# Optimization experiments

Hardware: AMD Instinct MI355X
Metric: run time of the kernel (lower is better)

Reference implementation:

```python
import jax, jax.numpy as jnp
import numpy as np
from itertools import product

_EPS = 1e-5
N_VOX = 120000
C = 64
B, D, H, Wd = 2, 400, 400, 40  # batch and spatial voxel grid


def _build_rulebook(seed=0):
    """Random unique active voxels + [N,27] submanifold neighbor index table (-1 = inactive)."""
    rng = np.random.default_rng(seed)
    size = B * D * H * Wd
    flat = rng.choice(size, size=N_VOX, replace=False)
    b = flat // (D * H * Wd)
    rem = flat % (D * H * Wd)
    z = rem // (H * Wd)
    rem2 = rem % (H * Wd)
    y = rem2 // Wd
    x = rem2 % Wd
    lut = np.full(size, -1, np.int32)
    lut[flat] = np.arange(N_VOX, dtype=np.int32)
    offs = np.array(list(product([-1, 0, 1], repeat=3)), dtype=np.int64)  # [27,3]
    zz = z[:, None] + offs[None, :, 0]
    yy = y[:, None] + offs[None, :, 1]
    xx = x[:, None] + offs[None, :, 2]
    valid = (zz >= 0) & (zz < D) & (yy >= 0) & (yy < H) & (xx >= 0) & (xx < Wd)
    nf = ((b[:, None] * D + zz) * H + yy) * Wd + xx
    nbr = np.where(valid, lut[np.clip(nf, 0, size - 1)], -1).astype(np.int32)
    return nbr


def setup_inputs() -> dict:
    key = jax.random.key(0)
    ks = jax.random.split(key, 12)
    nbr = jnp.asarray(_build_rulebook())
    return {
        "features": jax.random.normal(ks[0], (N_VOX, C), jnp.float32),
        "W1": jax.random.normal(ks[1], (27, C, C), jnp.float32) * 0.05,
        "g1": jax.random.uniform(ks[2], (C,), jnp.float32, 0.5, 1.5),
        "b1": jax.random.normal(ks[3], (C,), jnp.float32) * 0.1,
        "m1": jax.random.normal(ks[4], (C,), jnp.float32) * 0.1,
        "v1": jax.random.uniform(ks[5], (C,), jnp.float32, 0.5, 1.5),
        "W2": jax.random.normal(ks[6], (27, C, C), jnp.float32) * 0.05,
        "g2": jax.random.uniform(ks[7], (C,), jnp.float32, 0.5, 1.5),
        "b2": jax.random.normal(ks[8], (C,), jnp.float32) * 0.1,
        "m2": jax.random.normal(ks[9], (C,), jnp.float32) * 0.1,
        "v2": jax.random.uniform(ks[10], (C,), jnp.float32, 0.5, 1.5),
        "nbr_idx": nbr,
    }


def _subm_conv(f, nbr, W):
    # gather-GEMM: f [N,Cin], nbr [N,27], W [27,Cin,Cout] -> [N,Cout]
    mask = (nbr >= 0)[:, :, None]
    g = jnp.where(mask, f[jnp.clip(nbr, 0)], jnp.zeros((), f.dtype))  # [N,27,Cin]
    return jnp.einsum('nkc,kcd->nd', g, W)


def _bn(x, g, b, m, v):
    return (x - m) * (g * jax.lax.rsqrt(v + _EPS)) + b


def reference(features, W1, g1, b1, m1, v1, W2, g2, b2, m2, v2, nbr_idx):
    out = _bn(_subm_conv(features, nbr_idx, W1), g1, b1, m1, v1)
    out = jax.nn.relu(out)
    out = _bn(_subm_conv(out, nbr_idx, W2), g2, b2, m2, v2)
    return jax.nn.relu(out + features)
```

## Files before the change

kernel.cpp:

```cpp
#include <hip/hip_runtime.h>

typedef short short8 __attribute__((ext_vector_type(8)));
typedef float f32x4 __attribute__((ext_vector_type(4)));

#define N_VOX 120000
#define C64 64
#define K27 27
#define KC 13
#define TILES 3750
#define CAPT 64
#define LAYER_W 110592

#define WS_TCNT 0
#define WS_BNP  16384
#define WS_PWC  20480
#define WS_PWV  40960
#define WS_ENTS 524288
#define WS_MIDB (4u << 20)

__device__ __forceinline__ ushort f2bf(float x) {
    uint u = __float_as_uint(x);
    u = (u + 0x7FFFu + ((u >> 16) & 1u)) >> 16;
    return (ushort)u;
}
__device__ __forceinline__ float bf2f(ushort u) {
    return __uint_as_float((uint)u << 16);
}

__global__ __launch_bounds__(256) void prep_kernel(const float* __restrict__ W1,
                                                   const float* __restrict__ W2,
                                                   const float* g1, const float* b1,
                                                   const float* m1, const float* v1,
                                                   const float* g2, const float* b2,
                                                   const float* m2, const float* v2,
                                                   ushort* __restrict__ pwv,
                                                   ushort* __restrict__ pwc,
                                                   int* __restrict__ tcnt,
                                                   float* __restrict__ bnp) {
    int tid = blockIdx.x * 256 + threadIdx.x;
    if (tid < 221184) {
        int L = tid / LAYER_W, r = tid % LAYER_W;
        const float* W = L ? W2 : W1;
        pwv[tid] = f2bf(W[r]);
    } else if (tid < 229376) {
        int j2 = tid - 221184;
        int L = j2 >> 12, q = j2 & 4095;
        int ks = q >> 11, tq = (q >> 9) & 3, ln = (q >> 3) & 63, jj = q & 7;
        int c = ks * 32 + (ln >> 4) * 8 + jj;
        int d = tq * 16 + (ln & 15);
        const float* W = L ? W2 : W1;
        pwc[L * 4096 + q] = f2bf(W[(size_t)KC * 4096 + c * 64 + d]);
    } else if (tid < 233126) {
        tcnt[tid - 229376] = 0;
    } else if (tid < 233190) {
        int i = tid - 233126;
        float s1 = g1[i] * rsqrtf(v1[i] + 1e-5f);
        bnp[i] = s1; bnp[64 + i] = b1[i] - m1[i] * s1;
        float s2 = g2[i] * rsqrtf(v2[i] + 1e-5f);
        bnp[128 + i] = s2; bnp[192 + i] = b2[i] - m2[i] * s2;
    }
}

__global__ __launch_bounds__(256) void build_csr_kernel(const int* __restrict__ nbr,
                                                        int* __restrict__ tcnt,
                                                        int2* __restrict__ ents) {
    int n = blockIdx.x * 256 + threadIdx.x;
    if (n >= N_VOX) return;
    const int* row = nbr + (size_t)n * K27;
    const int tile = n >> 5, nl = n & 31;
#pragma unroll
    for (int k = 0; k < K27; ++k) {
        if (k == KC) continue;
        int m = row[k];
        if (m >= 0) {
            int slot = atomicAdd(&tcnt[tile], 1);
            if (slot < CAPT) ents[tile * CAPT + slot] = make_int2(nl | (k << 8), m);
        }
    }
}

template <bool LAYER2>
__global__ __launch_bounds__(64) void fused_layer_kernel(const float* __restrict__ f,
                                                         const ushort* __restrict__ midb_in,
                                                         const ushort* __restrict__ pwc,
                                                         const ushort* __restrict__ pwv,
                                                         const int* __restrict__ tcnt,
                                                         const int2* __restrict__ ents,
                                                         const float* __restrict__ bnp,
                                                         ushort* __restrict__ midb_out,
                                                         float* __restrict__ fout) {
    __shared__ float ext[32 * C64];
    const int lane = threadIdx.x;
    const int tile = blockIdx.x;
    const int n0 = tile * 32;
    const int r16 = lane & 15, kg = lane >> 4;

#pragma unroll
    for (int i = 0; i < 8; ++i) ((f32x4*)ext)[i * 64 + lane] = (f32x4)0.f;

    const short8* B = (const short8*)pwc;
    short8 Bf[2][4];
#pragma unroll
    for (int s = 0; s < 2; ++s)
#pragma unroll
        for (int t = 0; t < 4; ++t) Bf[s][t] = B[(s * 4 + t) * 64 + lane];

    f32x4 acc[2][4];
#pragma unroll
    for (int v = 0; v < 2; ++v)
#pragma unroll
        for (int t = 0; t < 4; ++t) acc[v][t] = (f32x4)0.f;

#pragma unroll
    for (int v = 0; v < 2; ++v) {
        short8 a0, a1;
        if (LAYER2) {
            const short8* ar = (const short8*)(midb_in + (size_t)(n0 + v * 16 + r16) * C64);
            a0 = ar[kg];
            a1 = ar[4 + kg];
        } else {
            const float4* ar = (const float4*)(f + (size_t)(n0 + v * 16 + r16) * C64);
            float4 fa = ar[kg * 2], fb = ar[kg * 2 + 1];
            float4 fc = ar[8 + kg * 2], fd = ar[9 + kg * 2];
            a0[0] = f2bf(fa.x); a0[1] = f2bf(fa.y); a0[2] = f2bf(fa.z); a0[3] = f2bf(fa.w);
            a0[4] = f2bf(fb.x); a0[5] = f2bf(fb.y); a0[6] = f2bf(fb.z); a0[7] = f2bf(fb.w);
            a1[0] = f2bf(fc.x); a1[1] = f2bf(fc.y); a1[2] = f2bf(fc.z); a1[3] = f2bf(fc.w);
            a1[4] = f2bf(fd.x); a1[5] = f2bf(fd.y); a1[6] = f2bf(fd.z); a1[7] = f2bf(fd.w);
        }
#pragma unroll
        for (int t = 0; t < 4; ++t) {
            acc[v][t] = __builtin_amdgcn_mfma_f32_16x16x32_bf16(a0, Bf[0][t], acc[v][t], 0, 0, 0);
            acc[v][t] = __builtin_amdgcn_mfma_f32_16x16x32_bf16(a1, Bf[1][t], acc[v][t], 0, 0, 0);
        }
    }

    int cnt = tcnt[tile];
    cnt = cnt > CAPT ? CAPT : cnt;
    for (int p = 0; p < cnt; ++p) {
        int2 e = ents[tile * CAPT + p];
        int nl = __builtin_amdgcn_readfirstlane(e.x & 255);
        int k  = __builtin_amdgcn_readfirstlane(e.x >> 8);
        int m  = __builtin_amdgcn_readfirstlane(e.y);
        const ushort* wk = pwv + (size_t)k * 4096 + lane;
        float ee = 0.f;
        if (LAYER2) {
            const ushort* am = midb_in + (size_t)m * C64;
#pragma unroll
            for (int c = 0; c < C64; ++c)
                ee = fmaf(bf2f(am[c]), bf2f(wk[c * 64]), ee);
        } else {
            const float* am = f + (size_t)m * C64;
#pragma unroll
            for (int c = 0; c < C64; ++c)
                ee = fmaf(am[c], bf2f(wk[c * 64]), ee);
        }
        ext[nl * C64 + lane] += ee;
    }

    float s[4], h[4];
#pragma unroll
    for (int t = 0; t < 4; ++t) {
        s[t] = bnp[t * 16 + r16];
        h[t] = bnp[64 + t * 16 + r16];
    }
#pragma unroll
    for (int v = 0; v < 2; ++v)
#pragma unroll
        for (int t = 0; t < 4; ++t)
#pragma unroll
            for (int r = 0; r < 4; ++r) {
                const int row = v * 16 + kg * 4 + r;
                const int ch = t * 16 + r16;
                float val = acc[v][t][r] + ext[row * C64 + ch];
                val = fmaf(val, s[t], h[t]);
                if (LAYER2) {
                    val += f[(size_t)(n0 + row) * C64 + ch];
                    fout[(size_t)(n0 + row) * C64 + ch] = fmaxf(val, 0.f);
                } else {
                    midb_out[(size_t)(n0 + row) * C64 + ch] = f2bf(fmaxf(val, 0.f));
                }
            }
}

extern "C" void kernel_launch(void* const* d_in, const int* in_sizes, int n_in,
                              void* d_out, int out_size, void* d_ws, size_t ws_size,
                              hipStream_t stream) {
    const float* f   = (const float*)d_in[0];
    const float* W1  = (const float*)d_in[1];
    const float* g1  = (const float*)d_in[2];
    const float* b1  = (const float*)d_in[3];
    const float* m1  = (const float*)d_in[4];
    const float* v1  = (const float*)d_in[5];
    const float* W2  = (const float*)d_in[6];
    const float* g2  = (const float*)d_in[7];
    const float* b2  = (const float*)d_in[8];
    const float* m2  = (const float*)d_in[9];
    const float* v2  = (const float*)d_in[10];
    const int*   nbr = (const int*)d_in[11];
    float* out = (float*)d_out;

    char* ws = (char*)d_ws;
    int*    tcnt = (int*)(ws + WS_TCNT);
    float*  bnp  = (float*)(ws + WS_BNP);
    ushort* pwc  = (ushort*)(ws + WS_PWC);
    ushort* pwv  = (ushort*)(ws + WS_PWV);
    int2*   ents = (int2*)(ws + WS_ENTS);
    ushort* midb = (ushort*)(ws + WS_MIDB);

    prep_kernel<<<911, 256, 0, stream>>>(W1, W2, g1, b1, m1, v1, g2, b2, m2, v2,
                                         pwv, pwc, tcnt, bnp);
    build_csr_kernel<<<(N_VOX + 255) / 256, 256, 0, stream>>>(nbr, tcnt, ents);

    fused_layer_kernel<false><<<TILES, 64, 0, stream>>>(
        f, nullptr, pwc, pwv, tcnt, ents, bnp, midb, nullptr);
    fused_layer_kernel<true><<<TILES, 64, 0, stream>>>(
        f, midb, pwc + 4096, pwv + LAYER_W, tcnt, ents, bnp + 128, nullptr, out);
}
```

Baseline: 183.5 us.

## Merge prep and CSR build, use LDS atomics, vectorize gathers and epilogue

Prep and CSR build now run in one launch. Each wave builds its tile's entry list with shared-memory atomics in place of global atomics, so the counter array no longer needs zeroing. The off-center weights are stored transposed, so each lane reads contiguous short8 rows, and the scalar dot product is split across four accumulators. The fused layer kernels pack four tiles per 256-thread block, and the epilogue goes through LDS so stores are coalesced float4/short8 writes. The risks are higher LDS use per block (32 KB), which limits occupancy, and more register pressure.

New measurement: 205.4 us. 1.12x slower.

```diff
diff --git a/kernel.cpp b/kernel.cpp
--- a/kernel.cpp
+++ b/kernel.cpp
@@ -10,11 +10,14 @@
 #define TILES 3750
 #define CAPT 64
 #define LAYER_W 110592
+#define CSRB 938
+#define PACKB 65
+#define FUSEB 938
 
 #define WS_TCNT 0
 #define WS_BNP  16384
 #define WS_PWC  20480
-#define WS_PWV  40960
+#define WS_PWT  40960
 #define WS_ENTS 524288
 #define WS_MIDB (4u << 20)
 
@@ -27,76 +30,84 @@
     return __uint_as_float((uint)u << 16);
 }
 
-__global__ __launch_bounds__(256) void prep_kernel(const float* __restrict__ W1,
-                                                   const float* __restrict__ W2,
-                                                   const float* g1, const float* b1,
-                                                   const float* m1, const float* v1,
-                                                   const float* g2, const float* b2,
-                                                   const float* m2, const float* v2,
-                                                   ushort* __restrict__ pwv,
-                                                   ushort* __restrict__ pwc,
-                                                   int* __restrict__ tcnt,
-                                                   float* __restrict__ bnp) {
-    int tid = blockIdx.x * 256 + threadIdx.x;
-    if (tid < 221184) {
-        int L = tid / LAYER_W, r = tid % LAYER_W;
-        const float* W = L ? W2 : W1;
-        pwv[tid] = f2bf(W[r]);
-    } else if (tid < 229376) {
-        int j2 = tid - 221184;
-        int L = j2 >> 12, q = j2 & 4095;
-        int ks = q >> 11, tq = (q >> 9) & 3, ln = (q >> 3) & 63, jj = q & 7;
-        int c = ks * 32 + (ln >> 4) * 8 + jj;
-        int d = tq * 16 + (ln & 15);
-        const float* W = L ? W2 : W1;
-        pwc[L * 4096 + q] = f2bf(W[(size_t)KC * 4096 + c * 64 + d]);
-    } else if (tid < 233126) {
-        tcnt[tid - 229376] = 0;
-    } else if (tid < 233190) {
-        int i = tid - 233126;
-        float s1 = g1[i] * rsqrtf(v1[i] + 1e-5f);
-        bnp[i] = s1; bnp[64 + i] = b1[i] - m1[i] * s1;
-        float s2 = g2[i] * rsqrtf(v2[i] + 1e-5f);
-        bnp[128 + i] = s2; bnp[192 + i] = b2[i] - m2[i] * s2;
-    }
-}
-
-__global__ __launch_bounds__(256) void build_csr_kernel(const int* __restrict__ nbr,
-                                                        int* __restrict__ tcnt,
-                                                        int2* __restrict__ ents) {
-    int n = blockIdx.x * 256 + threadIdx.x;
-    if (n >= N_VOX) return;
-    const int* row = nbr + (size_t)n * K27;
-    const int tile = n >> 5, nl = n & 31;
-#pragma unroll
-    for (int k = 0; k < K27; ++k) {
-        if (k == KC) continue;
-        int m = row[k];
-        if (m >= 0) {
-            int slot = atomicAdd(&tcnt[tile], 1);
-            if (slot < CAPT) ents[tile * CAPT + slot] = make_int2(nl | (k << 8), m);
-        }
-    }
-}
-
-template <bool LAYER2>
-__global__ __launch_bounds__(64) void fused_layer_kernel(const float* __restrict__ f,
-                                                         const ushort* __restrict__ midb_in,
-                                                         const ushort* __restrict__ pwc,
-                                                         const ushort* __restrict__ pwv,
-                                                         const int* __restrict__ tcnt,
-                                                         const int2* __restrict__ ents,
-                                                         const float* __restrict__ bnp,
-                                                         ushort* __restrict__ midb_out,
-                                                         float* __restrict__ fout) {
-    __shared__ float ext[32 * C64];
-    const int lane = threadIdx.x;
-    const int tile = blockIdx.x;
+__global__ __launch_bounds__(256) void prep_csr_kernel(
+    const int* __restrict__ nbr,
+    const float* __restrict__ W1, const float* __restrict__ W2,
+    const float* g1, const float* b1, const float* m1, const float* v1,
+    const float* g2, const float* b2, const float* m2, const float* v2,
+    int* __restrict__ tcnt, int2* __restrict__ ents,
+    ushort* __restrict__ pwt, ushort* __restrict__ pwc,
+    float* __restrict__ bnp) {
+    if (blockIdx.x < CSRB) {
+        __shared__ int cnt_[4];
+        const int wv = threadIdx.x >> 6, lane = threadIdx.x & 63;
+        const int tile = blockIdx.x * 4 + wv;
+        const bool act = tile < TILES;
+        if (lane == 0) cnt_[wv] = 0;
+        __syncthreads();
+        if (act) {
+            const int base = tile * (32 * K27);
+            for (int e = lane; e < 32 * K27; e += 64) {
+                const int k = e % K27;
+                if (k == KC) continue;
+                const int m = nbr[base + e];
+                if (m >= 0) {
+                    const int nl = e / K27;
+                    int slot = atomicAdd(&cnt_[wv], 1);
+                    if (slot < CAPT) ents[tile * CAPT + slot] = make_int2(nl | (k << 8), m);
+                }
+            }
+        }
+        __syncthreads();
+        if (act && lane == 0) {
+            int c = cnt_[wv];
+            tcnt[tile] = c > CAPT ? CAPT : c;
+        }
+    } else {
+        int idx = (blockIdx.x - CSRB) * 256 + threadIdx.x;
+        const int stride = PACKB * 256;
+        for (; idx < 229440; idx += stride) {
+            if (idx < 221184) {
+                int L = idx / LAYER_W, r = idx % LAYER_W;
+                int k = r >> 12, dc = r & 4095, d = dc >> 6, c = dc & 63;
+                const float* W = L ? W2 : W1;
+                pwt[idx] = f2bf(W[(size_t)k * 4096 + c * 64 + d]);
+            } else if (idx < 229376) {
+                int j2 = idx - 221184;
+                int L = j2 >> 12, q = j2 & 4095;
+                int ks = q >> 11, tq = (q >> 9) & 3, ln = (q >> 3) & 63, jj = q & 7;
+                int c = ks * 32 + (ln >> 4) * 8 + jj;
+                int d = tq * 16 + (ln & 15);
+                const float* W = L ? W2 : W1;
+                pwc[L * 4096 + q] = f2bf(W[(size_t)KC * 4096 + c * 64 + d]);
+            } else {
+                int i = idx - 229376;
+                float s1 = g1[i] * rsqrtf(v1[i] + 1e-5f);
+                bnp[i] = s1; bnp[64 + i] = b1[i] - m1[i] * s1;
+                float s2 = g2[i] * rsqrtf(v2[i] + 1e-5f);
+                bnp[128 + i] = s2; bnp[192 + i] = b2[i] - m2[i] * s2;
+            }
+        }
+    }
+}
+
+template <bool L2P>
+__device__ __forceinline__ void fused_core(const float* __restrict__ f,
+                                           const ushort* __restrict__ midin,
+                                           const ushort* __restrict__ pwc,
+                                           const ushort* __restrict__ pwt,
+                                           const int* __restrict__ tcnt,
+                                           const int2* __restrict__ ents,
+                                           const float* __restrict__ bnp,
+                                           ushort* __restrict__ midout,
+                                           float* __restrict__ fout,
+                                           float* exw, int tile) {
+    const int lane = threadIdx.x & 63;
+    const int r16 = lane & 15, kg = lane >> 4;
     const int n0 = tile * 32;
-    const int r16 = lane & 15, kg = lane >> 4;
-
-#pragma unroll
-    for (int i = 0; i < 8; ++i) ((f32x4*)ext)[i * 64 + lane] = (f32x4)0.f;
+
+#pragma unroll
+    for (int i = 0; i < 8; ++i) ((f32x4*)exw)[i * 64 + lane] = (f32x4)0.f;
 
     const short8* B = (const short8*)pwc;
     short8 Bf[2][4];
@@ -114,8 +125,8 @@
 #pragma unroll
     for (int v = 0; v < 2; ++v) {
         short8 a0, a1;
-        if (LAYER2) {
-            const short8* ar = (const short8*)(midb_in + (size_t)(n0 + v * 16 + r16) * C64);
+        if (L2P) {
+            const short8* ar = (const short8*)(midin + (size_t)(n0 + v * 16 + r16) * C64);
             a0 = ar[kg];
             a1 = ar[4 + kg];
         } else {
@@ -134,52 +145,123 @@
         }
     }
 
-    int cnt = tcnt[tile];
-    cnt = cnt > CAPT ? CAPT : cnt;
+    const int cnt = tcnt[tile];
     for (int p = 0; p < cnt; ++p) {
         int2 e = ents[tile * CAPT + p];
-        int nl = __builtin_amdgcn_readfirstlane(e.x & 255);
-        int k  = __builtin_amdgcn_readfirstlane(e.x >> 8);
-        int m  = __builtin_amdgcn_readfirstlane(e.y);
-        const ushort* wk = pwv + (size_t)k * 4096 + lane;
-        float ee = 0.f;
-        if (LAYER2) {
-            const ushort* am = midb_in + (size_t)m * C64;
-#pragma unroll
-            for (int c = 0; c < C64; ++c)
-                ee = fmaf(bf2f(am[c]), bf2f(wk[c * 64]), ee);
+        const int ex = __builtin_amdgcn_readfirstlane(e.x);
+        const int m  = __builtin_amdgcn_readfirstlane(e.y);
+        const int nl = ex & 255, k = ex >> 8;
+        const short8* wr = (const short8*)(pwt + (size_t)k * 4096 + lane * 64);
+        float ee0 = 0.f, ee1 = 0.f, ee2 = 0.f, ee3 = 0.f;
+        if (L2P) {
+            const uint* am = (const uint*)(midin + (size_t)m * C64);
+#pragma unroll
+            for (int g = 0; g < 8; ++g) {
+                short8 w8 = wr[g];
+                uint u0 = am[g * 4 + 0], u1 = am[g * 4 + 1];
+                uint u2 = am[g * 4 + 2], u3 = am[g * 4 + 3];
+                ee0 = fmaf(bf2f((ushort)u0),         bf2f((ushort)w8[0]), ee0);
+                ee1 = fmaf(bf2f((ushort)(u0 >> 16)), bf2f((ushort)w8[1]), ee1);
+                ee2 = fmaf(bf2f((ushort)u1),         bf2f((ushort)w8[2]), ee2);
+                ee3 = fmaf(bf2f((ushort)(u1 >> 16)), bf2f((ushort)w8[3]), ee3);
+                ee0 = fmaf(bf2f((ushort)u2),         bf2f((ushort)w8[4]), ee0);
+                ee1 = fmaf(bf2f((ushort)(u2 >> 16)), bf2f((ushort)w8[5]), ee1);
+                ee2 = fmaf(bf2f((ushort)u3),         bf2f((ushort)w8[6]), ee2);
+                ee3 = fmaf(bf2f((ushort)(u3 >> 16)), bf2f((ushort)w8[7]), ee3);
+            }
         } else {
-            const float* am = f + (size_t)m * C64;
-#pragma unroll
-            for (int c = 0; c < C64; ++c)
-                ee = fmaf(am[c], bf2f(wk[c * 64]), ee);
-        }
-        ext[nl * C64 + lane] += ee;
-    }
-
-    float s[4], h[4];
-#pragma unroll
-    for (int t = 0; t < 4; ++t) {
-        s[t] = bnp[t * 16 + r16];
-        h[t] = bnp[64 + t * 16 + r16];
-    }
+            const float4* am = (const float4*)(f + (size_t)m * C64);
+#pragma unroll
+            for (int g = 0; g < 8; ++g) {
+                short8 w8 = wr[g];
+                float4 x0 = am[g * 2], x1 = am[g * 2 + 1];
+                ee0 = fmaf(x0.x, bf2f((ushort)w8[0]), ee0);
+                ee1 = fmaf(x0.y, bf2f((ushort)w8[1]), ee1);
+                ee2 = fmaf(x0.z, bf2f((ushort)w8[2]), ee2);
+                ee3 = fmaf(x0.w, bf2f((ushort)w8[3]), ee3);
+                ee0 = fmaf(x1.x, bf2f((ushort)w8[4]), ee0);
+                ee1 = fmaf(x1.y, bf2f((ushort)w8[5]), ee1);
+                ee2 = fmaf(x1.z, bf2f((ushort)w8[6]), ee2);
+                ee3 = fmaf(x1.w, bf2f((ushort)w8[7]), ee3);
+            }
+        }
+        exw[nl * C64 + lane] += (ee0 + ee1) + (ee2 + ee3);
+    }
+
 #pragma unroll
     for (int v = 0; v < 2; ++v)
 #pragma unroll
         for (int t = 0; t < 4; ++t)
 #pragma unroll
-            for (int r = 0; r < 4; ++r) {
-                const int row = v * 16 + kg * 4 + r;
-                const int ch = t * 16 + r16;
-                float val = acc[v][t][r] + ext[row * C64 + ch];
-                val = fmaf(val, s[t], h[t]);
-                if (LAYER2) {
-                    val += f[(size_t)(n0 + row) * C64 + ch];
-                    fout[(size_t)(n0 + row) * C64 + ch] = fmaxf(val, 0.f);
-                } else {
-                    midb_out[(size_t)(n0 + row) * C64 + ch] = f2bf(fmaxf(val, 0.f));
-                }
-            }
+            for (int r = 0; r < 4; ++r)
+                exw[(v * 16 + kg * 4 + r) * C64 + t * 16 + r16] += acc[v][t][r];
+
+    const int row = lane >> 1, col0 = (lane & 1) * 32;
+    const f32x4* xl = (const f32x4*)(exw + row * C64 + col0);
+    const size_t gbase = (size_t)(n0 + row) * C64 + col0;
+    if (L2P) {
+#pragma unroll
+        for (int i = 0; i < 8; ++i) {
+            f32x4 x = xl[i];
+            float4 s  = *(const float4*)(bnp + col0 + i * 4);
+            float4 h  = *(const float4*)(bnp + 64 + col0 + i * 4);
+            float4 r4 = *(const float4*)(f + gbase + i * 4);
+            float4 o;
+            o.x = fmaxf(fmaf(x[0], s.x, h.x) + r4.x, 0.f);
+            o.y = fmaxf(fmaf(x[1], s.y, h.y) + r4.y, 0.f);
+            o.z = fmaxf(fmaf(x[2], s.z, h.z) + r4.z, 0.f);
+            o.w = fmaxf(fmaf(x[3], s.w, h.w) + r4.w, 0.f);
+            *(float4*)(fout + gbase + i * 4) = o;
+        }
+    } else {
+#pragma unroll
+        for (int i = 0; i < 4; ++i) {
+            f32x4 x0 = xl[i * 2], x1 = xl[i * 2 + 1];
+            float4 s0 = *(const float4*)(bnp + col0 + i * 8);
+            float4 s1 = *(const float4*)(bnp + col0 + i * 8 + 4);
+            float4 h0 = *(const float4*)(bnp + 64 + col0 + i * 8);
+            float4 h1 = *(const float4*)(bnp + 64 + col0 + i * 8 + 4);
+            short8 o;
+            o[0] = f2bf(fmaxf(fmaf(x0[0], s0.x, h0.x), 0.f));
+            o[1] = f2bf(fmaxf(fmaf(x0[1], s0.y, h0.y), 0.f));
+            o[2] = f2bf(fmaxf(fmaf(x0[2], s0.z, h0.z), 0.f));
+            o[3] = f2bf(fmaxf(fmaf(x0[3], s0.w, h0.w), 0.f));
+            o[4] = f2bf(fmaxf(fmaf(x1[0], s1.x, h1.x), 0.f));
+            o[5] = f2bf(fmaxf(fmaf(x1[1], s1.y, h1.y), 0.f));
+            o[6] = f2bf(fmaxf(fmaf(x1[2], s1.z, h1.z), 0.f));
+            o[7] = f2bf(fmaxf(fmaf(x1[3], s1.w, h1.w), 0.f));
+            *(short8*)(midout + gbase + i * 8) = o;
+        }
+    }
+}
+
+__global__ __launch_bounds__(256) void fused_l1_kernel(const float* __restrict__ f,
+                                                       const ushort* __restrict__ pwc,
+                                                       const ushort* __restrict__ pwt,
+                                                       const int* __restrict__ tcnt,
+                                                       const int2* __restrict__ ents,
+                                                       const float* __restrict__ bnp,
+                                                       ushort* __restrict__ midb) {
+    __shared__ float ext[4][32 * C64];
+    const int wv = threadIdx.x >> 6;
+    const int tile = blockIdx.x * 4 + wv;
+    if (tile >= TILES) return;
+    fused_core<false>(f, nullptr, pwc, pwt, tcnt, ents, bnp, midb, nullptr, ext[wv], tile);
+}
+
+__global__ __launch_bounds__(256) void fused_l2_kernel(const float* __restrict__ f,
+                                                       const ushort* __restrict__ midb,
+                                                       const ushort* __restrict__ pwc,
+                                                       const ushort* __restrict__ pwt,
+                                                       const int* __restrict__ tcnt,
+                                                       const int2* __restrict__ ents,
+                                                       const float* __restrict__ bnp,
+                                                       float* __restrict__ out) {
+    __shared__ float ext[4][32 * C64];
+    const int wv = threadIdx.x >> 6;
+    const int tile = blockIdx.x * 4 + wv;
+    if (tile >= TILES) return;
+    fused_core<true>(f, midb, pwc, pwt, tcnt, ents, bnp, nullptr, out, ext[wv], tile);
 }
 
 extern "C" void kernel_launch(void* const* d_in, const int* in_sizes, int n_in,
@@ -203,16 +285,14 @@
     int*    tcnt = (int*)(ws + WS_TCNT);
     float*  bnp  = (float*)(ws + WS_BNP);
     ushort* pwc  = (ushort*)(ws + WS_PWC);
-    ushort* pwv  = (ushort*)(ws + WS_PWV);
+    ushort* pwt  = (ushort*)(ws + WS_PWT);
     int2*   ents = (int2*)(ws + WS_ENTS);
     ushort* midb = (ushort*)(ws + WS_MIDB);
 
-    prep_kernel<<<911, 256, 0, stream>>>(W1, W2, g1, b1, m1, v1, g2, b2, m2, v2,
-                                         pwv, pwc, tcnt, bnp);
-    build_csr_kernel<<<(N_VOX + 255) / 256, 256, 0, stream>>>(nbr, tcnt, ents);
-
-    fused_layer_kernel<false><<<TILES, 64, 0, stream>>>(
-        f, nullptr, pwc, pwv, tcnt, ents, bnp, midb, nullptr);
-    fused_layer_kernel<true><<<TILES, 64, 0, stream>>>(
-        f, midb, pwc + 4096, pwv + LAYER_W, tcnt, ents, bnp + 128, nullptr, out);
-}
+    prep_csr_kernel<<<CSRB + PACKB, 256, 0, stream>>>(
+        nbr, W1, W2, g1, b1, m1, v1, g2, b2, m2, v2, tcnt, ents, pwt, pwc, bnp);
+
+    fused_l1_kernel<<<FUSEB, 256, 0, stream>>>(f, pwc, pwt, tcnt, ents, bnp, midb);
+    fused_l2_kernel<<<FUSEB, 256, 0, stream>>>(f, midb, pwc + 4096, pwt + LAYER_W,
+                                               tcnt, ents, bnp + 128, out);
+}
```
